# Kernel tuning notes

Hardware: AMD Instinct MI355X
Metric: run time of the kernel (lower is better)

Reference implementation:

```python
import jax, jax.numpy as jnp
import numpy as np

N_HEADS = 8
NEG_INF = -1e30  # finite stand-in for -inf in masked_fill (exact 0 prob after softmax)


def apply_rotary_emb(x, cos, sin):
    # x: [B, H, T, hd]; cos/sin: [T, hd] -> broadcast over B, H
    d = x.shape[-1]
    x1, x2 = x[..., : d // 2], x[..., d // 2 :]
    x_rot = jnp.concatenate((-x2, x1), axis=-1)
    return x * cos[None, None] + x_rot * sin[None, None]


def setup_inputs() -> dict:
    key = jax.random.key(0)
    ks = jax.random.split(key, 5)
    B, T, C, hd = 4, 2048, 512, 64
    x = jax.random.normal(ks[0], (B, T, C), dtype=jnp.float32)
    cos = jax.random.uniform(ks[1], (T, hd), dtype=jnp.float32)
    sin = jax.random.uniform(ks[2], (T, hd), dtype=jnp.float32)
    # xavier_uniform-ish scale for linear weights
    W_qkv = jax.random.normal(ks[3], (3 * C, C), dtype=jnp.float32) * (1.0 / np.sqrt(C))
    W_out = jax.random.normal(ks[4], (C, C), dtype=jnp.float32) * (1.0 / np.sqrt(C))
    return {"x": x, "cos": cos, "sin": sin, "W_qkv": W_qkv, "W_out": W_out}


def reference(x, cos, sin, W_qkv, W_out):
    B, T, C = x.shape
    H = N_HEADS
    hd = C // H
    # qkv projection (torch Linear: y = x @ W^T), split into q, k, v as [B, H, T, hd]
    qkv = (x @ W_qkv.T).reshape(B, T, 3, H, hd)
    qkv = jnp.transpose(qkv, (2, 0, 3, 1, 4))
    q, k, v = qkv[0], qkv[1], qkv[2]
    # RoPE on q, k
    q = apply_rotary_emb(q, cos[:T], sin[:T])
    k = apply_rotary_emb(k, cos[:T], sin[:T])
    scale = jnp.sqrt(jnp.float32(hd))
    attn = jnp.einsum("bhqd,bhkd->bhqk", q, k) / scale  # [B, H, T, T]
    causal = jnp.tril(jnp.ones((T, T), dtype=bool))
    attn = jnp.where(causal[None, None], attn, NEG_INF)
    attn = jax.nn.softmax(attn, axis=-1)
    out = jnp.einsum("bhqk,bhkd->bhqd", attn, v)  # [B, H, T, hd]
    out = jnp.transpose(out, (0, 2, 1, 3)).reshape(B, T, C)
    return out @ W_out.T
```

## Files before the change

kernel.cpp:

```cpp
#include <hip/hip_runtime.h>
#include <hip/hip_bf16.h>

#define B_SZ 4
#define T_SZ 2048
#define C_SZ 512
#define H_SZ 8
#define HD 64
#define QSCALE 0.1803368801111137f

typedef __bf16 bf16;
typedef __bf16 bf16x8 __attribute__((ext_vector_type(8)));
typedef float f32x4 __attribute__((ext_vector_type(4)));

__device__ __forceinline__ f32x4 mfma16(bf16x8 a, bf16x8 b, f32x4 c) {
    return __builtin_amdgcn_mfma_f32_16x16x32_bf16(a, b, c, 0, 0, 0);
}

#define GLD_LDS16(g, l) __builtin_amdgcn_global_load_lds( \
    (__attribute__((address_space(1))) void*)(void*)(g),  \
    (__attribute__((address_space(3))) void*)(l), 16, 0, 0)

__global__ __launch_bounds__(256) void cvt_all(
    const float* __restrict__ x, const float* __restrict__ wqkv,
    const float* __restrict__ wout, bf16* __restrict__ xb,
    bf16* __restrict__ wqb, bf16* __restrict__ wob) {
  int i = blockIdx.x * 256 + threadIdx.x;
  const int n0 = (B_SZ*T_SZ*C_SZ)/4, n1 = (3*C_SZ*C_SZ)/4, n2 = (C_SZ*C_SZ)/4;
  const float4* s; bf16* d; int j;
  if (i < n0)                { s = (const float4*)x;    d = xb;  j = i; }
  else if (i < n0 + n1)      { s = (const float4*)wqkv; d = wqb; j = i - n0; }
  else if (i < n0 + n1 + n2) { s = (const float4*)wout; d = wob; j = i - n0 - n1; }
  else return;
  float4 v = s[j];
  union { bf16 h[4]; uint2 u; } p;
  p.h[0] = (bf16)v.x; p.h[1] = (bf16)v.y; p.h[2] = (bf16)v.z; p.h[3] = (bf16)v.w;
  *(uint2*)(d + (size_t)j * 4) = p.u;
}

template<int EPI>
__global__ __launch_bounds__(256) void gemm_bt(
    const bf16* __restrict__ A, const bf16* __restrict__ Bw,
    int M, int N, int K,
    void* __restrict__ o0, void* __restrict__ o1, void* __restrict__ o2) {
  __shared__ bf16 sA[128 * 32];
  __shared__ bf16 sB[128 * 32];
  const int tid = threadIdx.x;
  const int m0 = blockIdx.x * 128, n0 = blockIdx.y * 128;
  const int w = tid >> 6, lane = tid & 63, quad = lane >> 4, l16 = lane & 15;
  const int wm = (w >> 1) * 64, wn = (w & 1) * 64;
  const int srow = tid >> 2, scol = (tid & 3) * 8;
  f32x4 acc[4][4] = {};
  for (int k0 = 0; k0 < K; k0 += 32) {
    __syncthreads();
    const bf16* ga = A  + (size_t)(m0 + srow) * K + k0 + scol;
    const bf16* gb = Bw + (size_t)(n0 + srow) * K + k0 + scol;
    GLD_LDS16(ga,                 sA + tid * 8);
    GLD_LDS16(ga + (size_t)64*K,  sA + tid * 8 + 2048);
    GLD_LDS16(gb,                 sB + tid * 8);
    GLD_LDS16(gb + (size_t)64*K,  sB + tid * 8 + 2048);
    __syncthreads();
    bf16x8 af[4], bfr[4];
#pragma unroll
    for (int i = 0; i < 4; i++)
      af[i] = *(const bf16x8*)(sA + (wm + i*16 + l16) * 32 + quad * 8);
#pragma unroll
    for (int j = 0; j < 4; j++)
      bfr[j] = *(const bf16x8*)(sB + (wn + j*16 + l16) * 32 + quad * 8);
#pragma unroll
    for (int i = 0; i < 4; i++)
#pragma unroll
      for (int j = 0; j < 4; j++)
        acc[i][j] = mfma16(af[i], bfr[j], acc[i][j]);
  }
  if (EPI == 0) {
    const int three = n0 >> 9;
    bf16* dst = three == 0 ? (bf16*)o0 : (three == 1 ? (bf16*)o1 : (bf16*)o2);
#pragma unroll
    for (int i = 0; i < 4; i++) {
#pragma unroll
      for (int j = 0; j < 4; j++) {
        const int n = n0 + wn + j*16 + l16;
        const int h = (n & 511) >> 6, dcol = n & 63;
#pragma unroll
        for (int r = 0; r < 4; r++) {
          const int m = m0 + wm + i*16 + quad*4 + r;
          const int b = m >> 11, t = m & (T_SZ - 1);
          if (three < 2)
            dst[(((size_t)(b*H_SZ + h)) * T_SZ + t) * HD + dcol] = (bf16)acc[i][j][r];
          else
            dst[(((size_t)(b*H_SZ + h)) * HD + dcol) * T_SZ + t] = (bf16)acc[i][j][r];
        }
      }
    }
  } else {
    float* dst = (float*)o0;
#pragma unroll
    for (int i = 0; i < 4; i++)
#pragma unroll
      for (int j = 0; j < 4; j++)
#pragma unroll
        for (int r = 0; r < 4; r++) {
          const int m = m0 + wm + i*16 + quad*4 + r;
          const int n = n0 + wn + j*16 + l16;
          dst[(size_t)m * N + n] = acc[i][j][r];
        }
  }
}

__global__ __launch_bounds__(256) void rope_qk(
    bf16* __restrict__ q, bf16* __restrict__ k,
    const float* __restrict__ cp, const float* __restrict__ sp) {
  const int i = blockIdx.x * 256 + threadIdx.x;
  const int d  = i & 31;
  const int t  = (i >> 5) & (T_SZ - 1);
  const int bh = i >> 16;
  const size_t base = ((size_t)bh * T_SZ + t) * HD;
  const float c1 = cp[t*HD + d], c2 = cp[t*HD + d + 32];
  const float s1 = sp[t*HD + d], s2 = sp[t*HD + d + 32];
  float a = (float)q[base + d], b = (float)q[base + d + 32];
  q[base + d]      = (bf16)((a * c1 - b * s1) * QSCALE);
  q[base + d + 32] = (bf16)((b * c2 + a * s2) * QSCALE);
  a = (float)k[base + d]; b = (float)k[base + d + 32];
  k[base + d]      = (bf16)(a * c1 - b * s1);
  k[base + d + 32] = (bf16)(b * c2 + a * s2);
}

__global__ __launch_bounds__(256) void flash_attn(
    const bf16* __restrict__ qb, const bf16* __restrict__ kb,
    const bf16* __restrict__ vtb, bf16* __restrict__ ao) {
  __shared__ bf16 sK[2][64 * 64];
  __shared__ bf16 sVT[2][64 * 64];
  __shared__ bf16 sP[4][2560];
  const int tid = threadIdx.x, w = tid >> 6, lane = tid & 63;
  const int quad = lane >> 4, l16 = lane & 15;
  const int bh = blockIdx.x & 31;
  const int pj = blockIdx.x >> 5;
  const int nA = (16 - pj) * 2;
  const int ntot = 34;
  int qi = 15 - pj;
  int q0w = qi * 128 + w * 32;
  const bf16* Q  = qb  + (size_t)bh * T_SZ * HD;
  const bf16* Kp = kb  + (size_t)bh * T_SZ * HD;
  const bf16* Vt = vtb + (size_t)bh * HD * T_SZ;
  bf16x8 qf[2][2];
#pragma unroll
  for (int nt = 0; nt < 2; nt++)
#pragma unroll
    for (int ds = 0; ds < 2; ds++)
      qf[nt][ds] = *(const bf16x8*)(Q + (size_t)(q0w + nt*16 + l16) * HD + ds*32 + quad*8);
  float l_[2] = {0.f, 0.f};
  f32x4 ot[4][2] = {};
  bf16* sPw = &sP[w][0];
  const int srow = tid >> 3, scg = (tid & 7) ^ (srow & 7);
  const int b = bh >> 3, h = bh & 7;

  auto epilogue = [&]() {
    float lt[2];
#pragma unroll
    for (int nt = 0; nt < 2; nt++) {
      float s = l_[nt];
      s += __shfl_xor(s, 16);
      s += __shfl_xor(s, 32);
      lt[nt] = 1.f / s;
    }
#pragma unroll
    for (int dt = 0; dt < 4; dt++)
#pragma unroll
      for (int nt = 0; nt < 2; nt++) {
        union { bf16 h4[4]; unsigned long long ull; } pk;
#pragma unroll
        for (int r = 0; r < 4; r++) pk.h4[r] = (bf16)(ot[dt][nt][r] * lt[nt]);
        *(unsigned long long*)(sPw + (nt*16 + l16)*72 + dt*16 + quad*4) = pk.ull;
      }
    asm volatile("" ::: "memory");
    const int oq = lane >> 1, half = lane & 1;
    const int tg = qi*128 + w*32 + oq;
    bf16* dst = ao + ((size_t)(b * T_SZ + tg)) * C_SZ + h * HD + half * 32;
#pragma unroll
    for (int j = 0; j < 4; j++)
      *(uint4*)(dst + j*8) = *(const uint4*)(sPw + oq*72 + half*32 + j*8);
    asm volatile("" ::: "memory");
  };

  GLD_LDS16(Kp + (size_t)srow * HD + scg*8,          sK[0]  + tid*8);
  GLD_LDS16(Kp + (size_t)(srow + 32) * HD + scg*8,   sK[0]  + tid*8 + 2048);
  GLD_LDS16(Vt + (size_t)srow * T_SZ + scg*8,        sVT[0] + tid*8);
  GLD_LDS16(Vt + (size_t)(srow + 32) * T_SZ + scg*8, sVT[0] + tid*8 + 2048);

  for (int it = 0; it < ntot; it++) {
    const int kt = (it < nA ? it : it - nA) * 64;
    __syncthreads();
    if (it + 1 < ntot) {
      const int kn = (it + 1 < nA ? it + 1 : it + 1 - nA) * 64;
      bf16* dK = sK[(it + 1) & 1];
      bf16* dV = sVT[(it + 1) & 1];
      GLD_LDS16(Kp + (size_t)(kn + srow) * HD + scg*8,        dK + tid*8);
      GLD_LDS16(Kp + (size_t)(kn + srow + 32) * HD + scg*8,   dK + tid*8 + 2048);
      GLD_LDS16(Vt + (size_t)srow * T_SZ + kn + scg*8,        dV + tid*8);
      GLD_LDS16(Vt + (size_t)(srow + 32) * T_SZ + kn + scg*8, dV + tid*8 + 2048);
    }
    if (kt <= q0w + 31) {
      const bf16* cK = sK[it & 1];
      const bf16* cV = sVT[it & 1];
      f32x4 st[4][2] = {};
#pragma unroll
      for (int mt = 0; mt < 4; mt++) {
#pragma unroll
        for (int ds = 0; ds < 2; ds++) {
          const int row = mt*16 + l16, cl = ds*4 + quad;
          const bf16x8 kf = *(const bf16x8*)(cK + row*64 + (cl ^ (row & 7)) * 8);
#pragma unroll
          for (int nt = 0; nt < 2; nt++)
            st[mt][nt] = mfma16(kf, qf[nt][ds], st[mt][nt]);
        }
      }
      if (kt + 63 > q0w) {
#pragma unroll
        for (int nt = 0; nt < 2; nt++) {
          const int qg = q0w + nt*16 + l16;
          const int kb0 = kt + quad*4;
#pragma unroll
          for (int mt = 0; mt < 4; mt++)
#pragma unroll
            for (int r = 0; r < 4; r++)
              st[mt][nt][r] = (kb0 + mt*16 + r <= qg) ? st[mt][nt][r] : -1e30f;
        }
      }
#pragma unroll
      for (int nt = 0; nt < 2; nt++) {
        float sum = 0.f;
#pragma unroll
        for (int mt = 0; mt < 4; mt++) {
          union { bf16 h4[4]; unsigned long long ull; } pk;
#pragma unroll
          for (int r = 0; r < 4; r++) {
            const float p = __builtin_amdgcn_exp2f(st[mt][nt][r]);
            sum += p;
            pk.h4[r] = (bf16)p;
          }
          *(unsigned long long*)(sPw + (mt>>1)*1280 + (nt*16 + l16)*40 + (mt&1)*16 + quad*4) = pk.ull;
        }
        l_[nt] += sum;
      }
      asm volatile("" ::: "memory");
      bf16x8 pf[2][2];
#pragma unroll
      for (int nt = 0; nt < 2; nt++)
#pragma unroll
        for (int s = 0; s < 2; s++)
          pf[nt][s] = *(const bf16x8*)(sPw + s*1280 + (nt*16 + l16)*40 + quad*8);
#pragma unroll
      for (int dt = 0; dt < 4; dt++) {
#pragma unroll
        for (int s = 0; s < 2; s++) {
          const int row = dt*16 + l16, cl = s*4 + quad;
          const bf16x8 vf = *(const bf16x8*)(cV + row*64 + (cl ^ (row & 7)) * 8);
#pragma unroll
          for (int nt = 0; nt < 2; nt++)
            ot[dt][nt] = mfma16(vf, pf[nt][s], ot[dt][nt]);
        }
      }
    }
    if (it == nA - 1) {
      epilogue();
      qi = pj; q0w = qi * 128 + w * 32;
#pragma unroll
      for (int nt = 0; nt < 2; nt++)
#pragma unroll
        for (int ds = 0; ds < 2; ds++)
          qf[nt][ds] = *(const bf16x8*)(Q + (size_t)(q0w + nt*16 + l16) * HD + ds*32 + quad*8);
      l_[0] = 0.f; l_[1] = 0.f;
#pragma unroll
      for (int dt = 0; dt < 4; dt++)
#pragma unroll
        for (int nt = 0; nt < 2; nt++)
          ot[dt][nt] = f32x4{0.f, 0.f, 0.f, 0.f};
    }
  }
  epilogue();
}

extern "C" void kernel_launch(void* const* d_in, const int* in_sizes, int n_in,
                              void* d_out, int out_size, void* d_ws, size_t ws_size,
                              hipStream_t stream) {
  const float* x    = (const float*)d_in[0];
  const float* cosp = (const float*)d_in[1];
  const float* sinp = (const float*)d_in[2];
  const float* wqkv = (const float*)d_in[3];
  const float* wout = (const float*)d_in[4];
  char* ws = (char*)d_ws;
  bf16* xb    = (bf16*)(ws);
  bf16* wqkvb = (bf16*)(ws +  8388608);
  bf16* woutb = (bf16*)(ws +  9961472);
  bf16* qbuf  = (bf16*)(ws + 10485760);
  bf16* kbuf  = (bf16*)(ws + 18874368);
  bf16* vtbuf = (bf16*)(ws + 27262976);
  bf16* ao    = (bf16*)(ws + 35651584);

  cvt_all<<<dim3(5120), dim3(256), 0, stream>>>(x, wqkv, wout, xb, wqkvb, woutb);
  gemm_bt<0><<<dim3(64, 12), dim3(256), 0, stream>>>(
      xb, wqkvb, B_SZ * T_SZ, 3 * C_SZ, C_SZ,
      (void*)qbuf, (void*)kbuf, (void*)vtbuf);
  rope_qk<<<dim3(8192), dim3(256), 0, stream>>>(qbuf, kbuf, cosp, sinp);
  flash_attn<<<dim3(256), dim3(256), 0, stream>>>(qbuf, kbuf, vtbuf, ao);
  gemm_bt<1><<<dim3(64, 4), dim3(256), 0, stream>>>(
      ao, woutb, B_SZ * T_SZ, C_SZ, C_SZ,
      (void*)d_out, nullptr, nullptr);
}
```

Baseline: 177.0 us.

## Fuse RoPE into QKV GEMM, split-K flash attention with combine, smaller out-GEMM tiles

```diff
diff --git a/kernel.cpp b/kernel.cpp
--- a/kernel.cpp
+++ b/kernel.cpp
@@ -1,5 +1,6 @@
 #include <hip/hip_runtime.h>
 #include <hip/hip_bf16.h>
+#include <math.h>
 
 #define B_SZ 4
 #define T_SZ 2048
@@ -37,11 +38,10 @@
   *(uint2*)(d + (size_t)j * 4) = p.u;
 }
 
-template<int EPI>
-__global__ __launch_bounds__(256) void gemm_bt(
+__global__ __launch_bounds__(256) void gemm_qkv(
     const bf16* __restrict__ A, const bf16* __restrict__ Bw,
-    int M, int N, int K,
-    void* __restrict__ o0, void* __restrict__ o1, void* __restrict__ o2) {
+    const float* __restrict__ cp, const float* __restrict__ sp,
+    bf16* __restrict__ oq, bf16* __restrict__ ok, bf16* __restrict__ ov) {
   __shared__ bf16 sA[128 * 32];
   __shared__ bf16 sB[128 * 32];
   const int tid = threadIdx.x;
@@ -49,6 +49,7 @@
   const int w = tid >> 6, lane = tid & 63, quad = lane >> 4, l16 = lane & 15;
   const int wm = (w >> 1) * 64, wn = (w & 1) * 64;
   const int srow = tid >> 2, scol = (tid & 3) * 8;
+  const int K = C_SZ;
   f32x4 acc[4][4] = {};
   for (int k0 = 0; k0 < K; k0 += 32) {
     __syncthreads();
@@ -72,11 +73,33 @@
       for (int j = 0; j < 4; j++)
         acc[i][j] = mfma16(af[i], bfr[j], acc[i][j]);
   }
-  if (EPI == 0) {
-    const int three = n0 >> 9;
-    bf16* dst = three == 0 ? (bf16*)o0 : (three == 1 ? (bf16*)o1 : (bf16*)o2);
-#pragma unroll
-    for (int i = 0; i < 4; i++) {
+  const int three = n0 >> 9;
+  if (three < 2) {
+    bf16* dst0 = three == 0 ? oq : ok;
+#pragma unroll
+    for (int i = 0; i < 4; i++)
+#pragma unroll
+      for (int r = 0; r < 4; r++) {
+        const int m = m0 + wm + i*16 + quad*4 + r;
+        const int b = m >> 11, t = m & (T_SZ - 1);
+#pragma unroll
+        for (int j = 0; j < 2; j++) {
+          const int dcol = j*16 + l16;
+          const int h = ((n0 & 511) + wn + dcol) >> 6;
+          const float c1 = cp[t*HD + dcol],     s1 = sp[t*HD + dcol];
+          const float c2 = cp[t*HD + dcol + 32], s2 = sp[t*HD + dcol + 32];
+          const float a = acc[i][j][r], bb = acc[i][j+2][r];
+          float o1 = a * c1 - bb * s1;
+          float o2 = bb * c2 + a * s2;
+          if (three == 0) { o1 *= QSCALE; o2 *= QSCALE; }
+          bf16* dst = dst0 + (((size_t)(b*H_SZ + h)) * T_SZ + t) * HD;
+          dst[dcol]      = (bf16)o1;
+          dst[dcol + 32] = (bf16)o2;
+        }
+      }
+  } else {
+#pragma unroll
+    for (int i = 0; i < 4; i++)
 #pragma unroll
       for (int j = 0; j < 4; j++) {
         const int n = n0 + wn + j*16 + l16;
@@ -85,59 +108,78 @@
         for (int r = 0; r < 4; r++) {
           const int m = m0 + wm + i*16 + quad*4 + r;
           const int b = m >> 11, t = m & (T_SZ - 1);
-          if (three < 2)
-            dst[(((size_t)(b*H_SZ + h)) * T_SZ + t) * HD + dcol] = (bf16)acc[i][j][r];
-          else
-            dst[(((size_t)(b*H_SZ + h)) * HD + dcol) * T_SZ + t] = (bf16)acc[i][j][r];
-        }
-      }
-    }
-  } else {
-    float* dst = (float*)o0;
-#pragma unroll
-    for (int i = 0; i < 4; i++)
+          ov[(((size_t)(b*H_SZ + h)) * HD + dcol) * T_SZ + t] = (bf16)acc[i][j][r];
+        }
+      }
+  }
+}
+
+__global__ __launch_bounds__(256) void gemm_out(
+    const bf16* __restrict__ A, const bf16* __restrict__ Bw,
+    float* __restrict__ dst) {
+  __shared__ bf16 sA[64 * 32];
+  __shared__ bf16 sB[128 * 32];
+  const int tid = threadIdx.x;
+  const int m0 = blockIdx.x * 64, n0 = blockIdx.y * 128;
+  const int w = tid >> 6, lane = tid & 63, quad = lane >> 4, l16 = lane & 15;
+  const int wm = (w & 1) * 32, wn = (w >> 1) * 64;
+  const int srow = tid >> 2, scol = (tid & 3) * 8;
+  const int K = C_SZ;
+  f32x4 acc[2][4] = {};
+  for (int k0 = 0; k0 < K; k0 += 32) {
+    __syncthreads();
+    const bf16* ga = A  + (size_t)(m0 + srow) * K + k0 + scol;
+    const bf16* gb = Bw + (size_t)(n0 + srow) * K + k0 + scol;
+    GLD_LDS16(ga,                 sA + tid * 8);
+    GLD_LDS16(gb,                 sB + tid * 8);
+    GLD_LDS16(gb + (size_t)64*K,  sB + tid * 8 + 2048);
+    __syncthreads();
+    bf16x8 af[2], bfr[4];
+#pragma unroll
+    for (int i = 0; i < 2; i++)
+      af[i] = *(const bf16x8*)(sA + (wm + i*16 + l16) * 32 + quad * 8);
+#pragma unroll
+    for (int j = 0; j < 4; j++)
+      bfr[j] = *(const bf16x8*)(sB + (wn + j*16 + l16) * 32 + quad * 8);
+#pragma unroll
+    for (int i = 0; i < 2; i++)
 #pragma unroll
       for (int j = 0; j < 4; j++)
-#pragma unroll
-        for (int r = 0; r < 4; r++) {
-          const int m = m0 + wm + i*16 + quad*4 + r;
-          const int n = n0 + wn + j*16 + l16;
-          dst[(size_t)m * N + n] = acc[i][j][r];
-        }
-  }
-}
-
-__global__ __launch_bounds__(256) void rope_qk(
-    bf16* __restrict__ q, bf16* __restrict__ k,
-    const float* __restrict__ cp, const float* __restrict__ sp) {
-  const int i = blockIdx.x * 256 + threadIdx.x;
-  const int d  = i & 31;
-  const int t  = (i >> 5) & (T_SZ - 1);
-  const int bh = i >> 16;
-  const size_t base = ((size_t)bh * T_SZ + t) * HD;
-  const float c1 = cp[t*HD + d], c2 = cp[t*HD + d + 32];
-  const float s1 = sp[t*HD + d], s2 = sp[t*HD + d + 32];
-  float a = (float)q[base + d], b = (float)q[base + d + 32];
-  q[base + d]      = (bf16)((a * c1 - b * s1) * QSCALE);
-  q[base + d + 32] = (bf16)((b * c2 + a * s2) * QSCALE);
-  a = (float)k[base + d]; b = (float)k[base + d + 32];
-  k[base + d]      = (bf16)(a * c1 - b * s1);
-  k[base + d + 32] = (bf16)(b * c2 + a * s2);
+        acc[i][j] = mfma16(af[i], bfr[j], acc[i][j]);
+  }
+#pragma unroll
+  for (int i = 0; i < 2; i++)
+#pragma unroll
+    for (int j = 0; j < 4; j++)
+#pragma unroll
+      for (int r = 0; r < 4; r++) {
+        const int m = m0 + wm + i*16 + quad*4 + r;
+        const int n = n0 + wn + j*16 + l16;
+        dst[(size_t)m * C_SZ + n] = acc[i][j][r];
+      }
+}
+
+__device__ __forceinline__ int tile_of(int g) {
+  int qi = (int)((sqrtf(4.f*(float)g + 1.f) - 1.f) * 0.5f);
+  while ((qi + 1) * (qi + 2) <= g) ++qi;
+  while (qi * (qi + 1) > g) --qi;
+  return qi;
 }
 
 __global__ __launch_bounds__(256) void flash_attn(
     const bf16* __restrict__ qb, const bf16* __restrict__ kb,
-    const bf16* __restrict__ vtb, bf16* __restrict__ ao) {
+    const bf16* __restrict__ vtb, bf16* __restrict__ Oa,
+    float* __restrict__ lbuf) {
   __shared__ bf16 sK[2][64 * 64];
   __shared__ bf16 sVT[2][64 * 64];
   __shared__ bf16 sP[4][2560];
   const int tid = threadIdx.x, w = tid >> 6, lane = tid & 63;
   const int quad = lane >> 4, l16 = lane & 15;
   const int bh = blockIdx.x & 31;
-  const int pj = blockIdx.x >> 5;
-  const int nA = (16 - pj) * 2;
-  const int ntot = 34;
-  int qi = 15 - pj;
+  const int p  = blockIdx.x >> 5;
+  const int gs = (34 * p) / 3, ge = (34 * (p + 1)) / 3;
+  int qi = tile_of(gs);
+  int tend = (qi + 1) * (qi + 2);
   int q0w = qi * 128 + w * 32;
   const bf16* Q  = qb  + (size_t)bh * T_SZ * HD;
   const bf16* Kp = kb  + (size_t)bh * T_SZ * HD;
@@ -152,16 +194,16 @@
   f32x4 ot[4][2] = {};
   bf16* sPw = &sP[w][0];
   const int srow = tid >> 3, scg = (tid & 7) ^ (srow & 7);
-  const int b = bh >> 3, h = bh & 7;
-
-  auto epilogue = [&]() {
-    float lt[2];
+
+  auto partial_epilogue = [&]() {
+    const int pf = (3 * qi * (qi + 1) + 2) / 34;
+    const int rec = (bh * 16 + qi) * 4 + (p - pf);
 #pragma unroll
     for (int nt = 0; nt < 2; nt++) {
       float s = l_[nt];
       s += __shfl_xor(s, 16);
       s += __shfl_xor(s, 32);
-      lt[nt] = 1.f / s;
+      if (quad == 0) lbuf[rec * 128 + w*32 + nt*16 + l16] = s;
     }
 #pragma unroll
     for (int dt = 0; dt < 4; dt++)
@@ -169,39 +211,44 @@
       for (int nt = 0; nt < 2; nt++) {
         union { bf16 h4[4]; unsigned long long ull; } pk;
 #pragma unroll
-        for (int r = 0; r < 4; r++) pk.h4[r] = (bf16)(ot[dt][nt][r] * lt[nt]);
+        for (int r = 0; r < 4; r++) pk.h4[r] = (bf16)ot[dt][nt][r];
         *(unsigned long long*)(sPw + (nt*16 + l16)*72 + dt*16 + quad*4) = pk.ull;
       }
     asm volatile("" ::: "memory");
-    const int oq = lane >> 1, half = lane & 1;
-    const int tg = qi*128 + w*32 + oq;
-    bf16* dst = ao + ((size_t)(b * T_SZ + tg)) * C_SZ + h * HD + half * 32;
+    const int oq = lane >> 1, hf = lane & 1;
+    bf16* dst = Oa + (size_t)rec * 8192 + (w*32 + oq) * 64 + hf * 32;
 #pragma unroll
     for (int j = 0; j < 4; j++)
-      *(uint4*)(dst + j*8) = *(const uint4*)(sPw + oq*72 + half*32 + j*8);
+      *(uint4*)(dst + j*8) = *(const uint4*)(sPw + oq*72 + hf*32 + j*8);
     asm volatile("" ::: "memory");
   };
 
-  GLD_LDS16(Kp + (size_t)srow * HD + scg*8,          sK[0]  + tid*8);
-  GLD_LDS16(Kp + (size_t)(srow + 32) * HD + scg*8,   sK[0]  + tid*8 + 2048);
-  GLD_LDS16(Vt + (size_t)srow * T_SZ + scg*8,        sVT[0] + tid*8);
-  GLD_LDS16(Vt + (size_t)(srow + 32) * T_SZ + scg*8, sVT[0] + tid*8 + 2048);
-
-  for (int it = 0; it < ntot; it++) {
-    const int kt = (it < nA ? it : it - nA) * 64;
-    __syncthreads();
-    if (it + 1 < ntot) {
-      const int kn = (it + 1 < nA ? it + 1 : it + 1 - nA) * 64;
-      bf16* dK = sK[(it + 1) & 1];
-      bf16* dV = sVT[(it + 1) & 1];
+  {
+    const int kt0 = (gs - qi * (qi + 1)) * 64;
+    bf16* dK = sK[gs & 1];
+    bf16* dV = sVT[gs & 1];
+    GLD_LDS16(Kp + (size_t)(kt0 + srow) * HD + scg*8,        dK + tid*8);
+    GLD_LDS16(Kp + (size_t)(kt0 + srow + 32) * HD + scg*8,   dK + tid*8 + 2048);
+    GLD_LDS16(Vt + (size_t)srow * T_SZ + kt0 + scg*8,        dV + tid*8);
+    GLD_LDS16(Vt + (size_t)(srow + 32) * T_SZ + kt0 + scg*8, dV + tid*8 + 2048);
+  }
+
+  for (int g = gs; g < ge; g++) {
+    const int kt = (g - qi * (qi + 1)) * 64;
+    __syncthreads();
+    if (g + 1 < ge) {
+      const int qn = (g + 1 >= tend) ? qi + 1 : qi;
+      const int kn = (g + 1 - qn * (qn + 1)) * 64;
+      bf16* dK = sK[(g + 1) & 1];
+      bf16* dV = sVT[(g + 1) & 1];
       GLD_LDS16(Kp + (size_t)(kn + srow) * HD + scg*8,        dK + tid*8);
       GLD_LDS16(Kp + (size_t)(kn + srow + 32) * HD + scg*8,   dK + tid*8 + 2048);
       GLD_LDS16(Vt + (size_t)srow * T_SZ + kn + scg*8,        dV + tid*8);
       GLD_LDS16(Vt + (size_t)(srow + 32) * T_SZ + kn + scg*8, dV + tid*8 + 2048);
     }
     if (kt <= q0w + 31) {
-      const bf16* cK = sK[it & 1];
-      const bf16* cV = sVT[it & 1];
+      const bf16* cK = sK[g & 1];
+      const bf16* cV = sVT[g & 1];
       f32x4 st[4][2] = {};
 #pragma unroll
       for (int mt = 0; mt < 4; mt++) {
@@ -234,21 +281,21 @@
           union { bf16 h4[4]; unsigned long long ull; } pk;
 #pragma unroll
           for (int r = 0; r < 4; r++) {
-            const float p = __builtin_amdgcn_exp2f(st[mt][nt][r]);
-            sum += p;
-            pk.h4[r] = (bf16)p;
+            const float pv = __builtin_amdgcn_exp2f(st[mt][nt][r]);
+            sum += pv;
+            pk.h4[r] = (bf16)pv;
           }
           *(unsigned long long*)(sPw + (mt>>1)*1280 + (nt*16 + l16)*40 + (mt&1)*16 + quad*4) = pk.ull;
         }
         l_[nt] += sum;
       }
       asm volatile("" ::: "memory");
-      bf16x8 pf[2][2];
+      bf16x8 pfr[2][2];
 #pragma unroll
       for (int nt = 0; nt < 2; nt++)
 #pragma unroll
         for (int s = 0; s < 2; s++)
-          pf[nt][s] = *(const bf16x8*)(sPw + s*1280 + (nt*16 + l16)*40 + quad*8);
+          pfr[nt][s] = *(const bf16x8*)(sPw + s*1280 + (nt*16 + l16)*40 + quad*8);
 #pragma unroll
       for (int dt = 0; dt < 4; dt++) {
 #pragma unroll
@@ -257,27 +304,65 @@
           const bf16x8 vf = *(const bf16x8*)(cV + row*64 + (cl ^ (row & 7)) * 8);
 #pragma unroll
           for (int nt = 0; nt < 2; nt++)
-            ot[dt][nt] = mfma16(vf, pf[nt][s], ot[dt][nt]);
-        }
-      }
-    }
-    if (it == nA - 1) {
-      epilogue();
-      qi = pj; q0w = qi * 128 + w * 32;
-#pragma unroll
-      for (int nt = 0; nt < 2; nt++)
-#pragma unroll
-        for (int ds = 0; ds < 2; ds++)
-          qf[nt][ds] = *(const bf16x8*)(Q + (size_t)(q0w + nt*16 + l16) * HD + ds*32 + quad*8);
-      l_[0] = 0.f; l_[1] = 0.f;
-#pragma unroll
-      for (int dt = 0; dt < 4; dt++)
+            ot[dt][nt] = mfma16(vf, pfr[nt][s], ot[dt][nt]);
+        }
+      }
+    }
+    if (g + 1 == tend || g + 1 == ge) {
+      partial_epilogue();
+      if (g + 1 == tend && g + 1 < ge) {
+        qi++; tend = (qi + 1) * (qi + 2); q0w = qi * 128 + w * 32;
 #pragma unroll
         for (int nt = 0; nt < 2; nt++)
-          ot[dt][nt] = f32x4{0.f, 0.f, 0.f, 0.f};
-    }
-  }
-  epilogue();
+#pragma unroll
+          for (int ds = 0; ds < 2; ds++)
+            qf[nt][ds] = *(const bf16x8*)(Q + (size_t)(q0w + nt*16 + l16) * HD + ds*32 + quad*8);
+        l_[0] = 0.f; l_[1] = 0.f;
+#pragma unroll
+        for (int dt = 0; dt < 4; dt++)
+#pragma unroll
+          for (int nt = 0; nt < 2; nt++)
+            ot[dt][nt] = f32x4{0.f, 0.f, 0.f, 0.f};
+      }
+    }
+  }
+}
+
+__global__ __launch_bounds__(256) void combine_o(
+    const bf16* __restrict__ Oa, const float* __restrict__ lbuf,
+    bf16* __restrict__ ao) {
+  const int inst = blockIdx.x;
+  const int bh = inst & 31, qi = inst >> 5;
+  const int b = bh >> 3, h = bh & 7;
+  const int g0 = qi * (qi + 1), geL = (qi + 1) * (qi + 2) - 1;
+  const int pf = (3 * g0 + 2) / 34, pl = (3 * geL + 2) / 34;
+  const int n = pl - pf + 1;
+  const int base = (bh * 16 + qi) * 4;
+  const int t = threadIdx.x;
+  const int q = t >> 1, d0 = (t & 1) * 32;
+  float l = 0.f;
+  for (int s = 0; s < n; s++) l += lbuf[(base + s) * 128 + q];
+  const float inv = 1.f / l;
+  float acc[32] = {};
+  for (int s = 0; s < n; s++) {
+    const bf16* ps = Oa + ((size_t)(base + s)) * 8192 + q * 64 + d0;
+#pragma unroll
+    for (int c = 0; c < 4; c++) {
+      union { uint4 u; bf16 h8[8]; } a;
+      a.u = *(const uint4*)(ps + c*8);
+#pragma unroll
+      for (int j = 0; j < 8; j++) acc[c*8 + j] += (float)a.h8[j];
+    }
+  }
+  const int tg = qi * 128 + q;
+  bf16* dst = ao + ((size_t)(b*T_SZ + tg)) * C_SZ + h*HD + d0;
+#pragma unroll
+  for (int c = 0; c < 4; c++) {
+    union { uint4 u; bf16 h8[8]; } o;
+#pragma unroll
+    for (int j = 0; j < 8; j++) o.h8[j] = (bf16)(acc[c*8 + j] * inv);
+    *(uint4*)(dst + c*8) = o.u;
+  }
 }
 
 extern "C" void kernel_launch(void* const* d_in, const int* in_sizes, int n_in,
@@ -296,14 +381,13 @@
   bf16* kbuf  = (bf16*)(ws + 18874368);
   bf16* vtbuf = (bf16*)(ws + 27262976);
   bf16* ao    = (bf16*)(ws + 35651584);
+  bf16* Oa    = (bf16*)(ws + 44040192);
+  float* lbuf = (float*)(ws + 77594624);
 
   cvt_all<<<dim3(5120), dim3(256), 0, stream>>>(x, wqkv, wout, xb, wqkvb, woutb);
-  gemm_bt<0><<<dim3(64, 12), dim3(256), 0, stream>>>(
-      xb, wqkvb, B_SZ * T_SZ, 3 * C_SZ, C_SZ,
-      (void*)qbuf, (void*)kbuf, (void*)vtbuf);
-  rope_qk<<<dim3(8192), dim3(256), 0, stream>>>(qbuf, kbuf, cosp, sinp);
-  flash_attn<<<dim3(256), dim3(256), 0, stream>>>(qbuf, kbuf, vtbuf, ao);
-  gemm_bt<1><<<dim3(64, 4), dim3(256), 0, stream>>>(
-      ao, woutb, B_SZ * T_SZ, C_SZ, C_SZ,
-      (void*)d_out, nullptr, nullptr);
-}
+  gemm_qkv<<<dim3(64, 12), dim3(256), 0, stream>>>(
+      xb, wqkvb, cosp, sinp, qbuf, kbuf, vtbuf);
+  flash_attn<<<dim3(768), dim3(256), 0, stream>>>(qbuf, kbuf, vtbuf, Oa, lbuf);
+  combine_o<<<dim3(512), dim3(256), 0, stream>>>(Oa, lbuf, ao);
+  gemm_out<<<dim3(128, 4), dim3(256), 0, stream>>>(ao, woutb, (float*)d_out);
+}
```

New measurement: 154.8 us. 12.5% less time.
